# Performance work log

Hardware: AMD Instinct MI355X
Metric: run time of the kernel (lower is better)

The kernel has to match this reference:

```python
import jax, jax.numpy as jnp
import numpy as np

B, T, C = 2, 1024, 1024
H, N = 16, 64
VOCAB = 32000
W_RANK, A_RANK, V_RANK, G_RANK = 64, 64, 32, 128
EPS_GN = 0.00064


def _wkv(r, w, k, v, a, b):
    # RWKV-7 per-token state recurrence. All args [B,T,C]; per-head state [N,N].
    Bq, Tq, Cq = r.shape
    def rs(u):
        return u.reshape(Bq, Tq, H, N).transpose(1, 0, 2, 3)  # [T,B,H,N]
    r_, k_, v_, a_, b_ = map(rs, (r, k, v, a, b))
    w_ = rs(jnp.exp(-jnp.exp(w.astype(jnp.float32))))  # decay in (0,1)
    def step(S, inp):
        rt, wt, kt, vt, at, bt = inp
        sa = jnp.einsum('bhij,bhj->bhi', S, at)
        S = S * wt[:, :, None, :] + jnp.einsum('bhi,bhj->bhij', sa, bt) + jnp.einsum('bhi,bhj->bhij', vt, kt)
        return S, jnp.einsum('bhij,bhj->bhi', S, rt)
    S0 = jnp.zeros((Bq, H, N, N), jnp.float32)
    _, out = jax.lax.scan(step, S0, (r_, w_, k_, v_, a_, b_))
    return out.transpose(1, 0, 2, 3).reshape(Bq, Tq, Cq).astype(r.dtype)


def _group_norm(x, weight, bias):
    # GroupNorm(H groups, C channels) over [B*T, C], eps=0.00064
    BT, Cq = x.shape
    xg = x.reshape(BT, H, Cq // H)
    mu = xg.mean(-1, keepdims=True)
    var = ((xg - mu) ** 2).mean(-1, keepdims=True)
    xn = ((xg - mu) / jnp.sqrt(var + EPS_GN)).reshape(BT, Cq)
    return xn * weight + bias


def setup_inputs() -> dict:
    key = jax.random.key(0)
    ks = iter(jax.random.split(key, 64))
    def nrm(shape, std):
        return jax.random.normal(next(ks), shape, jnp.float32) * std
    def xav(din, dout):
        return jax.random.normal(next(ks), (din, dout), jnp.float32) * np.float32(np.sqrt(2.0 / (din + dout)))
    inp = {}
    inp['x'] = jax.random.normal(next(ks), (B, T, C), jnp.float32)
    inp['rosa_ids'] = jax.random.randint(next(ks), (B, T), 0, VOCAB)
    for nm in ['x_r', 'x_w', 'x_k', 'x_v', 'x_a', 'x_g']:
        inp[nm] = nrm((1, 1, C), 0.01)
    for nm in ['w0', 'a0', 'v0']:
        inp[nm] = nrm((1, 1, C), 0.02)
    inp['w1'] = xav(C, W_RANK); inp['w2'] = xav(W_RANK, C)
    inp['a1'] = xav(C, A_RANK); inp['a2'] = xav(A_RANK, C)
    inp['v1'] = xav(C, V_RANK); inp['v2'] = xav(V_RANK, C)
    inp['g1'] = xav(C, G_RANK); inp['g2'] = xav(G_RANK, C)
    inp['k_k'] = 1.0 + nrm((1, 1, C), 0.02)
    inp['k_a'] = nrm((1, 1, C), 0.02)
    inp['r_k'] = nrm((H, N), 0.01)
    inp['Wr'] = xav(C, C); inp['Wk'] = xav(C, C); inp['Wv'] = xav(C, C); inp['Wo'] = xav(C, C)
    inp['ln_w'] = jnp.ones((C,), jnp.float32)
    inp['ln_b'] = jnp.zeros((C,), jnp.float32)
    inp['rosa_emb'] = nrm((VOCAB, C), 0.02)
    inp['rosa_gate'] = nrm((1, 1, C), 0.01)
    return inp


def reference(x, rosa_ids, x_r, x_w, x_k, x_v, x_a, x_g, w0, a0, v0,
              w1, w2, a1, a2, v1, v2, g1, g2, k_k, k_a, r_k,
              Wr, Wk, Wv, Wo, ln_w, ln_b, rosa_emb, rosa_gate):
    Bq, Tq, Cq = x.shape
    # time_shift: shift tokens right by one, zero-pad front
    xx = jnp.concatenate([jnp.zeros((Bq, 1, Cq), x.dtype), x[:, :-1]], axis=1) - x
    xr, xw, xk, xv, xa, xg = (x + xx * m for m in (x_r, x_w, x_k, x_v, x_a, x_g))
    r = xr @ Wr
    w = w0 + jnp.tanh(xw @ w1) @ w2
    k = xk @ Wk
    v = xv @ Wv
    # first-call v_first behavior: v_first = v.detach()
    v_first = jax.lax.stop_gradient(v)
    v = v + (v_first - v) * jax.nn.sigmoid(v0 + (xv @ v1) @ v2)
    a = jax.nn.sigmoid(a0 + (xa @ a1) @ a2)
    g = jax.nn.sigmoid(xg @ g1) @ g2
    kk = (k * k_k).reshape(Bq, Tq, H, N)
    kk = kk / jnp.maximum(jnp.linalg.norm(kk, axis=-1, keepdims=True), 1e-12)
    kk = kk.reshape(Bq, Tq, Cq)
    k = k * (1.0 + (a - 1.0) * k_a)
    o = _wkv(r, w, k, v, -kk, kk * a)
    o = _group_norm(o.reshape(Bq * Tq, Cq), ln_w, ln_b).reshape(Bq, Tq, Cq)
    rkv = ((r.reshape(Bq, Tq, H, N) * k.reshape(Bq, Tq, H, N) * r_k).sum(-1, keepdims=True)
           * v.reshape(Bq, Tq, H, N)).reshape(Bq, Tq, Cq)
    o = o + rkv
    emb = rosa_emb[rosa_ids]
    gate = jax.nn.sigmoid(o * rosa_gate).mean(-1, keepdims=True)
    o = o * (1.0 - gate) + emb * gate
    return (o * g) @ Wo
```

## Files before the change

kernel.cpp:

```cpp
#include <hip/hip_runtime.h>
#include <hip/hip_bf16.h>
#include <hip/hip_fp16.h>
#include <math.h>

constexpr int Bb = 2, Tt = 1024, Cc = 1024, Hh = 16, Nn = 64;
constexpr int Mtot = Bb * Tt;
constexpr int PACKW = 6 * Nn;
constexpr int SL_R = 0, SL_W = 1, SL_K = 2, SL_V = 3, SL_NK = 4, SL_BV = 5;
constexpr int PK2S = 768;

typedef _Float16 half8 __attribute__((ext_vector_type(8)));
typedef float f32x4 __attribute__((ext_vector_type(4)));
typedef unsigned int u32x4 __attribute__((ext_vector_type(4)));
typedef unsigned int u32x2 __attribute__((ext_vector_type(2)));

__device__ __forceinline__ float sigf(float x) { return 1.f / (1.f + expf(-x)); }

__device__ __forceinline__ unsigned short f2h(float f) {
    _Float16 h = (_Float16)f;
    return __builtin_bit_cast(unsigned short, h);
}
__device__ __forceinline__ float h2lo(unsigned int u) {
    return (float)__builtin_bit_cast(_Float16, (unsigned short)(u & 0xffffu));
}
__device__ __forceinline__ float h2hi(unsigned int u) {
    return (float)__builtin_bit_cast(_Float16, (unsigned short)(u >> 16));
}

__global__ __launch_bounds__(256) void mixcast_k(
    const float* __restrict__ x, const float* __restrict__ mr,
    const float* __restrict__ mk, const float* __restrict__ mv,
    const float* __restrict__ mw, const float* __restrict__ ma,
    const float* __restrict__ mg, unsigned short* __restrict__ xf)
{
    int idx = (blockIdx.x * 256 + threadIdx.x) * 4;
    int m = idx >> 10, c = idx & 1023;
    int t = m & (Tt - 1);
    float4 xc = *(const float4*)(x + idx);
    float4 xp = make_float4(0.f, 0.f, 0.f, 0.f);
    if (t) xp = *(const float4*)(x + idx - Cc);
    float4 d = make_float4(xp.x - xc.x, xp.y - xc.y, xp.z - xc.z, xp.w - xc.w);
    float4 m4;
    ushort4 o4;
#define EMIT(mixp, zoff)                                               \
    m4 = *(const float4*)(mixp + c);                                   \
    o4.x = f2h(xc.x + d.x * m4.x); o4.y = f2h(xc.y + d.y * m4.y);      \
    o4.z = f2h(xc.z + d.z * m4.z); o4.w = f2h(xc.w + d.w * m4.w);      \
    *(ushort4*)(xf + (size_t)(zoff)*2097152 + idx) = o4;
    EMIT(mr, 0)
    EMIT(mk, 1)
    EMIT(mv, 2)
    EMIT(mw, 3)
    EMIT(ma, 4)
    EMIT(mg, 5)
#undef EMIT
}

__global__ __launch_bounds__(256) void wtrans_k(
    const float* __restrict__ W0, const float* __restrict__ W1,
    const float* __restrict__ W2, const float* __restrict__ W3,
    unsigned short* __restrict__ WT)
{
    __shared__ float ls[64][65];
    const int z = blockIdx.z;
    const float* W = (z == 0) ? W0 : (z == 1) ? W1 : (z == 2) ? W2 : W3;
    unsigned short* dst = WT + (size_t)z * Cc * Cc;
    const int k0 = blockIdx.x * 64, n0 = blockIdx.y * 64;
    const int tid = threadIdx.x;
    const int rr = tid >> 4, c4 = tid & 15;
#pragma unroll
    for (int q = 0; q < 4; q++) {
        int kr = rr + q * 16;
        float4 v = *(const float4*)(W + (size_t)(k0 + kr) * Cc + n0 + c4 * 4);
        ls[kr][c4 * 4 + 0] = v.x; ls[kr][c4 * 4 + 1] = v.y;
        ls[kr][c4 * 4 + 2] = v.z; ls[kr][c4 * 4 + 3] = v.w;
    }
    __syncthreads();
#pragma unroll
    for (int q = 0; q < 4; q++) {
        int nr = rr + q * 16;
        ushort4 o;
        o.x = f2h(ls[c4 * 4 + 0][nr]);
        o.y = f2h(ls[c4 * 4 + 1][nr]);
        o.z = f2h(ls[c4 * 4 + 2][nr]);
        o.w = f2h(ls[c4 * 4 + 3][nr]);
        *(ushort4*)(dst + (size_t)(n0 + nr) * Cc + k0 + c4 * 4) = o;
    }
}

__global__ __launch_bounds__(256) void tr6_k(
    const float* __restrict__ w1, const float* __restrict__ a1, const float* __restrict__ g1,
    const float* __restrict__ w2, const float* __restrict__ a2, const float* __restrict__ g2,
    unsigned short* __restrict__ wts)
{
    int t = blockIdx.x;
    const float* src; unsigned short* dst; int R, C, tr, tc;
    if (t < 16)      { src = w1; dst = wts + 0;      R = 1024; C = 64;   tr = t;            tc = 0; }
    else if (t < 32) { src = a1; dst = wts + 65536;  R = 1024; C = 64;   tr = t - 16;       tc = 0; }
    else if (t < 64) { src = g1; dst = wts + 131072; R = 1024; C = 128;  tr = (t - 32) >> 1; tc = (t - 32) & 1; }
    else if (t < 80) { src = w2; dst = wts + 262144; R = 64;   C = 1024; tr = 0;            tc = t - 64; }
    else if (t < 96) { src = a2; dst = wts + 327680; R = 64;   C = 1024; tr = 0;            tc = t - 80; }
    else             { src = g2; dst = wts + 393216; R = 128;  C = 1024; tr = (t - 96) & 1; tc = (t - 96) >> 1; }
    __shared__ float ls[64][65];
    const int tid = threadIdx.x, rr = tid >> 4, c4 = tid & 15;
    const int r0 = tr * 64, c0 = tc * 64;
#pragma unroll
    for (int q = 0; q < 4; q++) {
        int r = rr + q * 16;
        float4 v = *(const float4*)(src + (size_t)(r0 + r) * C + c0 + c4 * 4);
        ls[r][c4 * 4 + 0] = v.x; ls[r][c4 * 4 + 1] = v.y;
        ls[r][c4 * 4 + 2] = v.z; ls[r][c4 * 4 + 3] = v.w;
    }
    __syncthreads();
#pragma unroll
    for (int q = 0; q < 4; q++) {
        int c = rr + q * 16;
        ushort4 o;
        o.x = f2h(ls[c4 * 4 + 0][c]);
        o.y = f2h(ls[c4 * 4 + 1][c]);
        o.z = f2h(ls[c4 * 4 + 2][c]);
        o.w = f2h(ls[c4 * 4 + 3][c]);
        *(ushort4*)(dst + (size_t)(c0 + c) * R + r0 + c4 * 4) = o;
    }
}

template <int RKV>
__global__ __launch_bounds__(256) void mgemm_k(
    const unsigned short* __restrict__ Abase, const unsigned short* __restrict__ WT,
    float* __restrict__ out, int M, int Ncol, int K)
{
    __shared__ unsigned short Ash[2][128][40];
    __shared__ unsigned short Bsh[2][64][40];
    const int z = RKV ? blockIdx.z : 0;
    const unsigned short* A = Abase + (size_t)z * 2097152;
    const unsigned short* BT = WT + (size_t)z * 1048576;
    const int tid = threadIdx.x;
    const int lane = tid & 63, wid = tid >> 6;
    const int wr = wid >> 1, wc = wid & 1;
    const int bm = blockIdx.y * 128, bn = blockIdx.x * 64;
    const int l15 = lane & 15, lk = lane >> 4;
    const int srow = tid >> 2, skc = tid & 3;

    f32x4 acc[4][2];
#pragma unroll
    for (int i = 0; i < 4; i++)
#pragma unroll
        for (int j = 0; j < 2; j++) acc[i][j] = (f32x4){0.f, 0.f, 0.f, 0.f};

    uint4 ra0, ra1, rb0;
    const size_t arow = (size_t)(bm + srow) * K + skc * 8;
    const size_t brow = (size_t)(bn + srow) * K + skc * 8;

#define LOADG(k0)                                                  \
    ra0 = *(const uint4*)(A + arow + (k0));                        \
    ra1 = *(const uint4*)(A + arow + (size_t)64 * K + (k0));       \
    rb0 = *(const uint4*)(BT + brow + (k0));
#define WRITEL(buf)                                                \
    *(uint4*)&Ash[buf][srow][skc * 8] = ra0;                       \
    *(uint4*)&Ash[buf][srow + 64][skc * 8] = ra1;                  \
    *(uint4*)&Bsh[buf][srow][skc * 8] = rb0;

    LOADG(0)
    WRITEL(0)
    __syncthreads();

    int cur = 0;
    for (int k0 = 0; k0 < K; k0 += 32) {
        const bool pf = (k0 + 32 < K);
        if (pf) { LOADG(k0 + 32) }
        half8 af[4], bf[2];
#pragma unroll
        for (int m = 0; m < 4; m++)
            af[m] = *(const half8*)&Ash[cur][wr * 64 + m * 16 + l15][lk * 8];
#pragma unroll
        for (int n = 0; n < 2; n++)
            bf[n] = *(const half8*)&Bsh[cur][wc * 32 + n * 16 + l15][lk * 8];
#pragma unroll
        for (int m = 0; m < 4; m++)
#pragma unroll
            for (int n = 0; n < 2; n++)
                acc[m][n] = __builtin_amdgcn_mfma_f32_16x16x32_f16(af[m], bf[n], acc[m][n], 0, 0, 0);
        if (pf) { WRITEL(cur ^ 1) }
        __syncthreads();
        cur ^= 1;
    }
#undef LOADG
#undef WRITEL

    const int slot = (z == 0) ? SL_R : (z == 1) ? SL_K : SL_V;
#pragma unroll
    for (int m = 0; m < 4; m++) {
#pragma unroll
        for (int n = 0; n < 2; n++) {
            int col = bn + wc * 32 + n * 16 + l15;
#pragma unroll
            for (int r = 0; r < 4; r++) {
                int row = bm + wr * 64 + m * 16 + lk * 4 + r;
                float cval = acc[m][n][r];
                if (RKV == 0) {
                    out[(size_t)row * Ncol + col] = cval;
                } else {
                    int b = row >> 10, t = row & (Tt - 1);
                    int h = col >> 6, nn2 = col & 63;
                    out[((size_t)(b * Hh + h) * Tt + t) * PACKW + slot * Nn + nn2] = cval;
                }
            }
        }
    }
}

__global__ __launch_bounds__(256) void lr1_k(
    const unsigned short* __restrict__ xf, const unsigned short* __restrict__ wts,
    unsigned short* __restrict__ h1)
{
    __shared__ unsigned short Ash[2][128][40];
    __shared__ unsigned short Bsh[2][64][40];
    const int bx = blockIdx.x;
    const unsigned short* A = xf + (size_t)(bx == 0 ? 3 : bx == 1 ? 4 : 5) * 2097152;
    const unsigned short* BT = wts + (bx == 0 ? 0 : bx == 1 ? 65536 : 131072 + (bx - 2) * 65536);
    const int colbase = bx * 64;
    const int K = 1024;
    const int tid = threadIdx.x;
    const int lane = tid & 63, wid = tid >> 6;
    const int wr = wid >> 1, wc = wid & 1;
    const int bm = blockIdx.y * 128;
    const int l15 = lane & 15, lk = lane >> 4;
    const int srow = tid >> 2, skc = tid & 3;

    f32x4 acc[4][2];
#pragma unroll
    for (int i = 0; i < 4; i++)
#pragma unroll
        for (int j = 0; j < 2; j++) acc[i][j] = (f32x4){0.f, 0.f, 0.f, 0.f};

    uint4 ra0, ra1, rb0;
    const size_t arow = (size_t)(bm + srow) * K + skc * 8;
    const size_t brow = (size_t)srow * K + skc * 8;

#define LOADG(k0)                                                  \
    ra0 = *(const uint4*)(A + arow + (k0));                        \
    ra1 = *(const uint4*)(A + arow + (size_t)64 * K + (k0));       \
    rb0 = *(const uint4*)(BT + brow + (k0));
#define WRITEL(buf)                                                \
    *(uint4*)&Ash[buf][srow][skc * 8] = ra0;                       \
    *(uint4*)&Ash[buf][srow + 64][skc * 8] = ra1;                  \
    *(uint4*)&Bsh[buf][srow][skc * 8] = rb0;

    LOADG(0)
    WRITEL(0)
    __syncthreads();

    int cur = 0;
    for (int k0 = 0; k0 < K; k0 += 32) {
        const bool pf = (k0 + 32 < K);
        if (pf) { LOADG(k0 + 32) }
        half8 af[4], bf[2];
#pragma unroll
        for (int m = 0; m < 4; m++)
            af[m] = *(const half8*)&Ash[cur][wr * 64 + m * 16 + l15][lk * 8];
#pragma unroll
        for (int n = 0; n < 2; n++)
            bf[n] = *(const half8*)&Bsh[cur][wc * 32 + n * 16 + l15][lk * 8];
#pragma unroll
        for (int m = 0; m < 4; m++)
#pragma unroll
            for (int n = 0; n < 2; n++)
                acc[m][n] = __builtin_amdgcn_mfma_f32_16x16x32_f16(af[m], bf[n], acc[m][n], 0, 0, 0);
        if (pf) { WRITEL(cur ^ 1) }
        __syncthreads();
        cur ^= 1;
    }
#undef LOADG
#undef WRITEL

#pragma unroll
    for (int m = 0; m < 4; m++) {
#pragma unroll
        for (int n = 0; n < 2; n++) {
            int col = colbase + wc * 32 + n * 16 + l15;
#pragma unroll
            for (int r = 0; r < 4; r++) {
                int row = bm + wr * 64 + m * 16 + lk * 4 + r;
                float c = acc[m][n][r];
                if (bx == 0) c = tanhf(c);
                else if (bx >= 2) c = sigf(c);
                h1[(size_t)row * 256 + col] = f2h(c);
            }
        }
    }
}

__global__ __launch_bounds__(256) void lr2_k(
    const unsigned short* __restrict__ h1, const unsigned short* __restrict__ wts,
    const float* __restrict__ w0, const float* __restrict__ a0,
    float* __restrict__ pack, float* __restrict__ gbuf)
{
    __shared__ unsigned short Ash[128][40];
    __shared__ unsigned short Bsh[64][40];
    const int z = blockIdx.z;
    const int K = (z == 2) ? 128 : 64;
    const int aoff = (z == 0) ? 0 : (z == 1) ? 64 : 128;
    const unsigned short* BT = wts + 262144 + z * 65536;
    const int tid = threadIdx.x;
    const int lane = tid & 63, wid = tid >> 6;
    const int wr = wid >> 1, wc = wid & 1;
    const int bm = blockIdx.y * 128, bn = blockIdx.x * 64;
    const int l15 = lane & 15, lk = lane >> 4;
    const int srow = tid >> 2, skc = tid & 3;

    f32x4 acc[4][2];
#pragma unroll
    for (int i = 0; i < 4; i++)
#pragma unroll
        for (int j = 0; j < 2; j++) acc[i][j] = (f32x4){0.f, 0.f, 0.f, 0.f};

    for (int k0 = 0; k0 < K; k0 += 32) {
        uint4 ra0 = *(const uint4*)(h1 + (size_t)(bm + srow) * 256 + aoff + k0 + skc * 8);
        uint4 ra1 = *(const uint4*)(h1 + (size_t)(bm + srow + 64) * 256 + aoff + k0 + skc * 8);
        uint4 rb0 = *(const uint4*)(BT + (size_t)(bn + srow) * K + k0 + skc * 8);
        *(uint4*)&Ash[srow][skc * 8] = ra0;
        *(uint4*)&Ash[srow + 64][skc * 8] = ra1;
        *(uint4*)&Bsh[srow][skc * 8] = rb0;
        __syncthreads();
        half8 af[4], bf[2];
#pragma unroll
        for (int m = 0; m < 4; m++)
            af[m] = *(const half8*)&Ash[wr * 64 + m * 16 + l15][lk * 8];
#pragma unroll
        for (int n = 0; n < 2; n++)
            bf[n] = *(const half8*)&Bsh[wc * 32 + n * 16 + l15][lk * 8];
#pragma unroll
        for (int m = 0; m < 4; m++)
#pragma unroll
            for (int n = 0; n < 2; n++)
                acc[m][n] = __builtin_amdgcn_mfma_f32_16x16x32_f16(af[m], bf[n], acc[m][n], 0, 0, 0);
        __syncthreads();
    }

#pragma unroll
    for (int m = 0; m < 4; m++) {
#pragma unroll
        for (int n = 0; n < 2; n++) {
            int col = bn + wc * 32 + n * 16 + l15;
#pragma unroll
            for (int r = 0; r < 4; r++) {
                int row = bm + wr * 64 + m * 16 + lk * 4 + r;
                float c = acc[m][n][r];
                int b = row >> 10, t = row & (Tt - 1);
                int h = col >> 6, nn2 = col & 63;
                if (z == 0) {
                    pack[((size_t)(b * Hh + h) * Tt + t) * PACKW + SL_W * Nn + nn2] = expf(-expf(w0[col] + c));
                } else if (z == 1) {
                    pack[((size_t)(b * Hh + h) * Tt + t) * PACKW + SL_BV * Nn + nn2] = sigf(a0[col] + c);
                } else {
                    gbuf[(size_t)row * Cc + col] = c;
                }
            }
        }
    }
}

__global__ __launch_bounds__(256) void prep_k(float* __restrict__ pk,
                                              unsigned char* __restrict__ pk2,
                                              const float* __restrict__ k_k,
                                              const float* __restrict__ k_a)
{
    int inst = blockIdx.x * 4 + (threadIdx.x >> 6);
    int lane = threadIdx.x & 63;
    int b = inst >> 14;
    int rem = inst & 16383;
    int t = rem >> 4;
    int h = rem & 15;
    size_t base = ((size_t)(b * Hh + h) * Tt + t) * PACKW;
    int c = h * 64 + lane;
    float rv   = pk[base + SL_R * 64 + lane];
    float wv   = pk[base + SL_W * 64 + lane];
    float kraw = pk[base + SL_K * 64 + lane];
    float vv   = pk[base + SL_V * 64 + lane];
    float a    = pk[base + SL_BV * 64 + lane];
    float kkv = kraw * k_k[c];
    float ss = kkv * kkv;
#pragma unroll
    for (int m = 1; m < 64; m <<= 1) ss += __shfl_xor(ss, m);
    float kkn = kkv / fmaxf(sqrtf(ss), 1e-12f);
    float kmod = kraw * (1.f + (a - 1.f) * k_a[c]);
    pk[base + SL_K * 64 + lane] = kmod;

    unsigned char* sb = pk2 + ((size_t)(b * Hh + h) * Tt + t) * PK2S;
    *(unsigned int*)(sb + lane * 4)       = (unsigned)f2h(rv) | ((unsigned)f2h(kmod) << 16);
    *(unsigned int*)(sb + 256 + lane * 4) = (unsigned)f2h(-kkn) | ((unsigned)f2h(kkn * a) << 16);
    *(unsigned short*)(sb + 512 + lane * 2) = f2h(wv);
    *(unsigned short*)(sb + 640 + lane * 2) = f2h(vv);
}

template <int C>
__device__ __forceinline__ float dppmov(float x) {
    return __int_as_float(__builtin_amdgcn_mov_dpp(__float_as_int(x), C, 0xF, 0xF, 1));
}
__device__ __forceinline__ float red16(float v) {
    v += dppmov<0xB1>(v);
    v += dppmov<0x4E>(v);
    v += dppmov<0x141>(v);
    v += dppmov<0x140>(v);
    return v;
}

struct Slot { u32x4 a; u32x4 b; u32x2 w; unsigned int v; };

__device__ __forceinline__ void stepf6(float4& S, const Slot& f, int jb, float* optr)
{
    float r0 = h2lo(f.a[0]), k0 = h2hi(f.a[0]);
    float r1 = h2lo(f.a[1]), k1 = h2hi(f.a[1]);
    float r2 = h2lo(f.a[2]), k2 = h2hi(f.a[2]);
    float r3 = h2lo(f.a[3]), k3 = h2hi(f.a[3]);
    float n0 = h2lo(f.b[0]), b0 = h2hi(f.b[0]);
    float n1 = h2lo(f.b[1]), b1 = h2hi(f.b[1]);
    float n2 = h2lo(f.b[2]), b2 = h2hi(f.b[2]);
    float n3 = h2lo(f.b[3]), b3 = h2hi(f.b[3]);
    float w0 = h2lo(f.w[0]), w1 = h2hi(f.w[0]);
    float w2f = h2lo(f.w[1]), w3 = h2hi(f.w[1]);
    float vv = h2lo(f.v);
    float p0 = fmaf(S.y, n1, S.x * n0);
    float p1 = fmaf(S.w, n3, S.z * n2);
    float sa = red16(p0 + p1);
    S.x = fmaf(S.x, w0, fmaf(sa, b0, vv * k0));
    S.y = fmaf(S.y, w1, fmaf(sa, b1, vv * k1));
    S.z = fmaf(S.z, w2f, fmaf(sa, b2, vv * k2));
    S.w = fmaf(S.w, w3, fmaf(sa, b3, vv * k3));
    float q0 = fmaf(S.y, r1, S.x * r0);
    float q1 = fmaf(S.w, r3, S.z * r2);
    float ot = red16(q0 + q1);
    if (jb == 0) *optr = ot;
}

__global__ __launch_bounds__(64, 1) void wkv_k(const unsigned char* __restrict__ pk2,
                                               float* __restrict__ o)
{
    const int bx = blockIdx.x;
    const int xcd = bx & 7;
    const int ix = bx >> 3;
    const int bh = ((ix >> 4) << 3) | xcd;
    const int rg = ix & 15;
    const int lane = threadIdx.x;
    const int ri = lane >> 4;
    const int jb = lane & 15;
    const int i = rg * 4 + ri;
    const int b = bh >> 4, h = bh & 15;
    const unsigned char* base = pk2 + (size_t)bh * Tt * PK2S;
    const unsigned char* p1 = base + jb * 16;
    const unsigned char* p2 = base + 512 + jb * 8;
    const unsigned char* p3 = base + 640 + i * 2;
    float* ob = o + (size_t)b * Tt * Cc + h * 64 + i;

    Slot sl[8];

#define ISSUE(s, Q1, Q2, Q3)                                                                              \
    asm volatile("global_load_dwordx4 %0, %1, off"            : "=v"(sl[s].a) : "v"(Q1) : "memory");      \
    asm volatile("global_load_dwordx4 %0, %1, off offset:256" : "=v"(sl[s].b) : "v"(Q1) : "memory");      \
    asm volatile("global_load_dwordx2 %0, %1, off"            : "=v"(sl[s].w) : "v"(Q2) : "memory");      \
    asm volatile("global_load_ushort %0, %1, off"             : "=v"(sl[s].v) : "v"(Q3) : "memory");

    ISSUE(0, p1 + 0 * PK2S, p2 + 0 * PK2S, p3 + 0 * PK2S)
    ISSUE(1, p1 + 1 * PK2S, p2 + 1 * PK2S, p3 + 1 * PK2S)
    ISSUE(2, p1 + 2 * PK2S, p2 + 2 * PK2S, p3 + 2 * PK2S)
    ISSUE(3, p1 + 3 * PK2S, p2 + 3 * PK2S, p3 + 3 * PK2S)
    ISSUE(4, p1 + 4 * PK2S, p2 + 4 * PK2S, p3 + 4 * PK2S)
    ISSUE(5, p1 + 5 * PK2S, p2 + 5 * PK2S, p3 + 5 * PK2S)
    ISSUE(6, p1 + 6 * PK2S, p2 + 6 * PK2S, p3 + 6 * PK2S)
    ISSUE(7, p1 + 7 * PK2S, p2 + 7 * PK2S, p3 + 7 * PK2S)

    const unsigned char* q1 = p1 + 8 * PK2S;
    const unsigned char* q2 = p2 + 8 * PK2S;
    const unsigned char* q3 = p3 + 8 * PK2S;
    float4 S = make_float4(0.f, 0.f, 0.f, 0.f);

#define STEP(u)                                                          \
    asm volatile("s_waitcnt vmcnt(28)" ::: "memory");                    \
    __builtin_amdgcn_sched_barrier(0);                                   \
    stepf6(S, sl[u], jb, ob + (size_t)(t0 + (u)) * Cc);                  \
    ISSUE(u, q1, q2, q3)                                                 \
    if (t0 + (u) + 9 < Tt) { q1 += PK2S; q2 += PK2S; q3 += PK2S; }

    for (int t0 = 0; t0 < Tt; t0 += 8) {
        STEP(0) STEP(1) STEP(2) STEP(3) STEP(4) STEP(5) STEP(6) STEP(7)
    }
#undef STEP
#undef ISSUE
}

__global__ __launch_bounds__(256) void post_k(
    const float* __restrict__ o, const float* __restrict__ pk, const float* __restrict__ gbuf,
    const float* __restrict__ r_k, const float* __restrict__ ln_w, const float* __restrict__ ln_b,
    const int* __restrict__ ids, const float* __restrict__ emb, const float* __restrict__ rgate,
    unsigned short* __restrict__ outh)
{
    __shared__ float sred[4];
    const int bt = blockIdx.x;
    const int b = bt >> 10, t = bt & 1023;
    const int tid = threadIdx.x;
    const int c0 = tid * 4;
    const int h = tid >> 4;
    const int nn = c0 & 63;

    float4 o4 = *(const float4*)(o + (size_t)bt * Cc + c0);
    float s = o4.x + o4.y + o4.z + o4.w;
    float ss = o4.x * o4.x + o4.y * o4.y + o4.z * o4.z + o4.w * o4.w;
#pragma unroll
    for (int m = 1; m < 16; m <<= 1) { s += __shfl_xor(s, m); ss += __shfl_xor(ss, m); }
    float mu = s * (1.f / 64.f);
    float inv = rsqrtf(ss * (1.f / 64.f) - mu * mu + 0.00064f);

    size_t pbase = ((size_t)(b * Hh + h) * Tt + t) * PACKW;
    float4 r4 = *(const float4*)(pk + pbase + SL_R * 64 + nn);
    float4 k4 = *(const float4*)(pk + pbase + SL_K * 64 + nn);
    float4 v4 = *(const float4*)(pk + pbase + SL_V * 64 + nn);
    float4 q4 = *(const float4*)(r_k + h * 64 + nn);
    float dot = r4.x * k4.x * q4.x + r4.y * k4.y * q4.y + r4.z * k4.z * q4.z + r4.w * k4.w * q4.w;
#pragma unroll
    for (int m = 1; m < 16; m <<= 1) dot += __shfl_xor(dot, m);

    float4 lw = *(const float4*)(ln_w + c0);
    float4 lb = *(const float4*)(ln_b + c0);
    float e0 = (o4.x - mu) * inv * lw.x + lb.x + dot * v4.x;
    float e1 = (o4.y - mu) * inv * lw.y + lb.y + dot * v4.y;
    float e2 = (o4.z - mu) * inv * lw.z + lb.z + dot * v4.z;
    float e3 = (o4.w - mu) * inv * lw.w + lb.w + dot * v4.w;

    float4 rg4 = *(const float4*)(rgate + c0);
    float gp = sigf(e0 * rg4.x) + sigf(e1 * rg4.y) + sigf(e2 * rg4.z) + sigf(e3 * rg4.w);
#pragma unroll
    for (int m = 1; m < 64; m <<= 1) gp += __shfl_xor(gp, m);
    if ((tid & 63) == 0) sred[tid >> 6] = gp;
    __syncthreads();
    float gate = (sred[0] + sred[1] + sred[2] + sred[3]) * (1.f / 1024.f);

    const int id = ids[bt];
    float4 em = *(const float4*)(emb + (size_t)id * Cc + c0);
    float4 g4 = *(const float4*)(gbuf + (size_t)bt * Cc + c0);
    ushort4 h4;
    h4.x = f2h((e0 * (1.f - gate) + em.x * gate) * g4.x);
    h4.y = f2h((e1 * (1.f - gate) + em.y * gate) * g4.y);
    h4.z = f2h((e2 * (1.f - gate) + em.z * gate) * g4.z);
    h4.w = f2h((e3 * (1.f - gate) + em.w * gate) * g4.w);
    *(ushort4*)(outh + (size_t)bt * Cc + c0) = h4;
}

extern "C" void kernel_launch(void* const* d_in, const int* in_sizes, int n_in,
                              void* d_out, int out_size, void* d_ws, size_t ws_size,
                              hipStream_t stream)
{
    (void)in_sizes; (void)n_in; (void)out_size; (void)ws_size;
    const float* x    = (const float*)d_in[0];
    const int*   ids  = (const int*)d_in[1];
    const float* x_r  = (const float*)d_in[2];
    const float* x_w  = (const float*)d_in[3];
    const float* x_k  = (const float*)d_in[4];
    const float* x_v  = (const float*)d_in[5];
    const float* x_a  = (const float*)d_in[6];
    const float* x_g  = (const float*)d_in[7];
    const float* w0   = (const float*)d_in[8];
    const float* a0   = (const float*)d_in[9];
    const float* w1   = (const float*)d_in[11];
    const float* w2   = (const float*)d_in[12];
    const float* a1   = (const float*)d_in[13];
    const float* a2   = (const float*)d_in[14];
    const float* g1   = (const float*)d_in[17];
    const float* g2   = (const float*)d_in[18];
    const float* k_k  = (const float*)d_in[19];
    const float* k_a  = (const float*)d_in[20];
    const float* r_k  = (const float*)d_in[21];
    const float* Wr   = (const float*)d_in[22];
    const float* Wk   = (const float*)d_in[23];
    const float* Wv   = (const float*)d_in[24];
    const float* Wo   = (const float*)d_in[25];
    const float* ln_w = (const float*)d_in[26];
    const float* ln_b = (const float*)d_in[27];
    const float* emb  = (const float*)d_in[28];
    const float* rg   = (const float*)d_in[29];

    float* ws = (float*)d_ws;
    float* pack = ws;
    float* obuf = pack + (size_t)12582912;
    float* gbuf = obuf + (size_t)2097152;
    unsigned short* xf  = (unsigned short*)(gbuf + (size_t)2097152);
    unsigned short* wt  = xf + (size_t)6 * 2097152;
    unsigned short* wts = wt + (size_t)4 * 1048576;
    unsigned short* h1  = wts + (size_t)524288;
    unsigned short* obh = xf;
    unsigned char*  pk2 = (unsigned char*)(xf + (size_t)2097152);

    dim3 blk(256);

    wtrans_k<<<dim3(16, 16, 4), blk, 0, stream>>>(Wr, Wk, Wv, Wo, wt);
    tr6_k<<<dim3(128), blk, 0, stream>>>(w1, a1, g1, w2, a2, g2, wts);
    mixcast_k<<<dim3(2048), blk, 0, stream>>>(x, x_r, x_k, x_v, x_w, x_a, x_g, xf);

    mgemm_k<1><<<dim3(Cc / 64, Mtot / 128, 3), blk, 0, stream>>>(xf, wt, pack, Mtot, Cc, Cc);
    lr1_k<<<dim3(4, 16), blk, 0, stream>>>(xf, wts, h1);
    lr2_k<<<dim3(16, 16, 3), blk, 0, stream>>>(h1, wts, w0, a0, pack, gbuf);

    prep_k<<<dim3(Bb * Tt * Hh / 4), blk, 0, stream>>>(pack, pk2, k_k, k_a);
    wkv_k<<<dim3(512), dim3(64), 0, stream>>>(pk2, obuf);
    post_k<<<dim3(Mtot), blk, 0, stream>>>(obuf, pack, gbuf, r_k, ln_w, ln_b, ids, emb, rg, obh);
    mgemm_k<0><<<dim3(Cc / 64, Mtot / 128, 1), blk, 0, stream>>>(obh, wt + (size_t)3 * 1048576, (float*)d_out, Mtot, Cc, Cc);
}
```

Baseline: 260.6 us.

## Split WKV state across 32 lanes per row and double block count

Each lane of the WKV recurrence kernel now holds two state elements instead of four, so 32 lanes cover a row and each wave handles two rows. The grid doubles to 1024 single-wave blocks, and the block-to-head mapping changes to match. Per-lane loads shrink (dwordx2/dword instead of dwordx4/dwordx2), and fewer FMAs sit on each step's critical path. In exchange, each row reduction needs an extra ds_swizzle cross-half exchange on top of the DPP steps, which lengthens the serial per-token latency chain. Total load traffic also rises because r/k/a/b are fetched by twice as many waves.

```diff
diff --git a/kernel.cpp b/kernel.cpp
--- a/kernel.cpp
+++ b/kernel.cpp
@@ -11,7 +11,6 @@
 
 typedef _Float16 half8 __attribute__((ext_vector_type(8)));
 typedef float f32x4 __attribute__((ext_vector_type(4)));
-typedef unsigned int u32x4 __attribute__((ext_vector_type(4)));
 typedef unsigned int u32x2 __attribute__((ext_vector_type(2)));
 
 __device__ __forceinline__ float sigf(float x) { return 1.f / (1.f + expf(-x)); }
@@ -397,39 +396,31 @@
 __device__ __forceinline__ float dppmov(float x) {
     return __int_as_float(__builtin_amdgcn_mov_dpp(__float_as_int(x), C, 0xF, 0xF, 1));
 }
-__device__ __forceinline__ float red16(float v) {
+__device__ __forceinline__ float red32(float v) {
     v += dppmov<0xB1>(v);
     v += dppmov<0x4E>(v);
     v += dppmov<0x141>(v);
     v += dppmov<0x140>(v);
+    v += __int_as_float(__builtin_amdgcn_ds_swizzle(__float_as_int(v), 0x401F));
     return v;
 }
 
-struct Slot { u32x4 a; u32x4 b; u32x2 w; unsigned int v; };
-
-__device__ __forceinline__ void stepf6(float4& S, const Slot& f, int jb, float* optr)
+struct Slot { u32x2 a; u32x2 b; unsigned int w; unsigned int v; };
+
+__device__ __forceinline__ void stepv(float& S0, float& S1, const Slot& f, int jb, float* optr)
 {
     float r0 = h2lo(f.a[0]), k0 = h2hi(f.a[0]);
     float r1 = h2lo(f.a[1]), k1 = h2hi(f.a[1]);
-    float r2 = h2lo(f.a[2]), k2 = h2hi(f.a[2]);
-    float r3 = h2lo(f.a[3]), k3 = h2hi(f.a[3]);
     float n0 = h2lo(f.b[0]), b0 = h2hi(f.b[0]);
     float n1 = h2lo(f.b[1]), b1 = h2hi(f.b[1]);
-    float n2 = h2lo(f.b[2]), b2 = h2hi(f.b[2]);
-    float n3 = h2lo(f.b[3]), b3 = h2hi(f.b[3]);
-    float w0 = h2lo(f.w[0]), w1 = h2hi(f.w[0]);
-    float w2f = h2lo(f.w[1]), w3 = h2hi(f.w[1]);
+    float w0 = h2lo(f.w), w1 = h2hi(f.w);
     float vv = h2lo(f.v);
-    float p0 = fmaf(S.y, n1, S.x * n0);
-    float p1 = fmaf(S.w, n3, S.z * n2);
-    float sa = red16(p0 + p1);
-    S.x = fmaf(S.x, w0, fmaf(sa, b0, vv * k0));
-    S.y = fmaf(S.y, w1, fmaf(sa, b1, vv * k1));
-    S.z = fmaf(S.z, w2f, fmaf(sa, b2, vv * k2));
-    S.w = fmaf(S.w, w3, fmaf(sa, b3, vv * k3));
-    float q0 = fmaf(S.y, r1, S.x * r0);
-    float q1 = fmaf(S.w, r3, S.z * r2);
-    float ot = red16(q0 + q1);
+    float sa = fmaf(S1, n1, S0 * n0);
+    sa = red32(sa);
+    S0 = fmaf(S0, w0, fmaf(sa, b0, vv * k0));
+    S1 = fmaf(S1, w1, fmaf(sa, b1, vv * k1));
+    float ot = fmaf(S1, r1, S0 * r0);
+    ot = red32(ot);
     if (jb == 0) *optr = ot;
 }
 
@@ -439,25 +430,25 @@
     const int bx = blockIdx.x;
     const int xcd = bx & 7;
     const int ix = bx >> 3;
-    const int bh = ((ix >> 4) << 3) | xcd;
-    const int rg = ix & 15;
+    const int bh = xcd * 4 + (ix >> 5);
+    const int rg = ix & 31;
     const int lane = threadIdx.x;
-    const int ri = lane >> 4;
-    const int jb = lane & 15;
-    const int i = rg * 4 + ri;
+    const int ri = lane >> 5;
+    const int jb = lane & 31;
+    const int i = rg * 2 + ri;
     const int b = bh >> 4, h = bh & 15;
     const unsigned char* base = pk2 + (size_t)bh * Tt * PK2S;
-    const unsigned char* p1 = base + jb * 16;
-    const unsigned char* p2 = base + 512 + jb * 8;
+    const unsigned char* p1 = base + jb * 8;
+    const unsigned char* p2 = base + 512 + jb * 4;
     const unsigned char* p3 = base + 640 + i * 2;
     float* ob = o + (size_t)b * Tt * Cc + h * 64 + i;
 
     Slot sl[8];
 
 #define ISSUE(s, Q1, Q2, Q3)                                                                              \
-    asm volatile("global_load_dwordx4 %0, %1, off"            : "=v"(sl[s].a) : "v"(Q1) : "memory");      \
-    asm volatile("global_load_dwordx4 %0, %1, off offset:256" : "=v"(sl[s].b) : "v"(Q1) : "memory");      \
-    asm volatile("global_load_dwordx2 %0, %1, off"            : "=v"(sl[s].w) : "v"(Q2) : "memory");      \
+    asm volatile("global_load_dwordx2 %0, %1, off"            : "=v"(sl[s].a) : "v"(Q1) : "memory");      \
+    asm volatile("global_load_dwordx2 %0, %1, off offset:256" : "=v"(sl[s].b) : "v"(Q1) : "memory");      \
+    asm volatile("global_load_dword %0, %1, off"              : "=v"(sl[s].w) : "v"(Q2) : "memory");      \
     asm volatile("global_load_ushort %0, %1, off"             : "=v"(sl[s].v) : "v"(Q3) : "memory");
 
     ISSUE(0, p1 + 0 * PK2S, p2 + 0 * PK2S, p3 + 0 * PK2S)
@@ -472,12 +463,12 @@
     const unsigned char* q1 = p1 + 8 * PK2S;
     const unsigned char* q2 = p2 + 8 * PK2S;
     const unsigned char* q3 = p3 + 8 * PK2S;
-    float4 S = make_float4(0.f, 0.f, 0.f, 0.f);
+    float S0 = 0.f, S1 = 0.f;
 
 #define STEP(u)                                                          \
     asm volatile("s_waitcnt vmcnt(28)" ::: "memory");                    \
     __builtin_amdgcn_sched_barrier(0);                                   \
-    stepf6(S, sl[u], jb, ob + (size_t)(t0 + (u)) * Cc);                  \
+    stepv(S0, S1, sl[u], jb, ob + (size_t)(t0 + (u)) * Cc);              \
     ISSUE(u, q1, q2, q3)                                                 \
     if (t0 + (u) + 9 < Tt) { q1 += PK2S; q2 += PK2S; q3 += PK2S; }
 
@@ -600,7 +591,7 @@
     lr2_k<<<dim3(16, 16, 3), blk, 0, stream>>>(h1, wts, w0, a0, pack, gbuf);
 
     prep_k<<<dim3(Bb * Tt * Hh / 4), blk, 0, stream>>>(pack, pk2, k_k, k_a);
-    wkv_k<<<dim3(512), dim3(64), 0, stream>>>(pk2, obuf);
+    wkv_k<<<dim3(1024), dim3(64), 0, stream>>>(pk2, obuf);
     post_k<<<dim3(Mtot), blk, 0, stream>>>(obuf, pack, gbuf, r_k, ln_w, ln_b, ids, emb, rg, obh);
     mgemm_k<0><<<dim3(Cc / 64, Mtot / 128, 1), blk, 0, stream>>>(obh, wt + (size_t)3 * 1048576, (float*)d_out, Mtot, Cc, Cc);
 }
```

Result: slower. 302.6 us (+16.1%).
